# Kernel optimization log

Measured on AMD Instinct MI355X. Metric: run time of the kernel, lower is better.

## Reference

```python
import jax, jax.numpy as jnp
import numpy as np

D_IN, D_HIDDEN, DT_RANK = 768, 16, 48


def setup_inputs() -> dict:
    key = jax.random.key(0)
    ks = jax.random.split(key, 6)
    b, l, d, n, r = 2, 2048, D_IN, D_HIDDEN, DT_RANK
    p = 3 * n + 2 * d + 2 * r  # x_proj output width = 1680
    x = jax.random.normal(ks[0], (b, l, d), jnp.float32)
    z = jax.random.normal(ks[1], (b, d, l), jnp.float32)
    # A_log = log(repeat(arange(1, n+1), 'n -> d n'))
    A_log = jnp.log(jnp.broadcast_to(jnp.arange(1, n + 1, dtype=jnp.float32), (d, n)))
    D = jnp.ones((d,), jnp.float32)
    W_xproj = jax.random.normal(ks[2], (p, d), jnp.float32) / np.sqrt(d)
    W_dt = jax.random.normal(ks[3], (d, r), jnp.float32) / np.sqrt(r)
    # dt bias init: inverse-softplus of dt ~ LogUniform(1e-3, 1e-1)
    dt = jnp.exp(jax.random.uniform(ks[4], (d,)) * (np.log(0.1) - np.log(0.001)) + np.log(0.001))
    dt = jnp.clip(dt, 1e-4)
    b_dt = dt + jnp.log(-jnp.expm1(-dt))
    return dict(x=x, z=z, A_log=A_log, D=D, W_xproj=W_xproj, W_dt=W_dt, b_dt=b_dt)


def reference(x, z, A_log, D, W_xproj, W_dt, b_dt):
    b, l, d = x.shape
    n = A_log.shape[1]
    r = W_dt.shape[1]
    A = -jnp.exp(A_log)                      # (d, n)
    proj = x @ W_xproj.T                     # (b, l, 3n + 2d + 2r)
    Bm = proj[..., :n]                       # (b, l, n)  input matrix B
    Cm = proj[..., 2 * n:3 * n]              # (b, l, n)  output matrix C
    dt = proj[..., 3 * n + 2 * d:3 * n + 2 * d + r]   # (b, l, r)
    # NOTE: source adds dt_proj bias via the Linear AND again via delta_bias -> 2*b_dt
    delta = jax.nn.softplus(dt @ W_dt.T + 2.0 * b_dt)  # (b, l, d)
    dA = jnp.exp(delta[..., None] * A)                  # (b, l, d, n)
    dBu = (delta * x)[..., None] * Bm[:, :, None, :]    # (b, l, d, n)

    def step(h, inp):
        dA_t, dBu_t, C_t = inp
        h = dA_t * h + dBu_t                 # (b, d, n)
        return h, jnp.einsum('bdn,bn->bd', h, C_t)

    h0 = jnp.zeros((b, d, n), x.dtype)
    _, ys = jax.lax.scan(step, h0, (jnp.swapaxes(dA, 0, 1), jnp.swapaxes(dBu, 0, 1), jnp.swapaxes(Cm, 0, 1)))
    y = jnp.swapaxes(ys, 0, 1) + x * D       # (b, l, d)  + skip D*u
    zl = jnp.swapaxes(z, 1, 2)               # z is (b, d, l) -> (b, l, d)
    return y * (zl * jax.nn.sigmoid(zl))     # gate with silu(z)
```

## Files before the change

### kernel.cpp

```cpp
#include <hip/hip_runtime.h>
#include <math.h>

#define BATCH 2
#define LSEQ  2048
#define DIM   768
#define NST   16
#define RDT   48
#define BL    (BATCH*LSEQ)
#define NCHUNK 32
#define CLEN   (LSEQ/NCHUNK)
#define CPAD   68
#define NPACK  (CLEN/4)
#define LP4    (LSEQ/4)
#define L2E    1.4426950408889634f

typedef __attribute__((ext_vector_type(8))) short short8;
typedef __attribute__((ext_vector_type(4))) float float4e;

__device__ __forceinline__ ushort f2bf(float f) {
    union { float f; unsigned u; } v; v.f = f;
    unsigned u = v.u;
    u += 0x7fffu + ((u >> 16) & 1u);
    return (ushort)(u >> 16);
}

template <int CTRL>
__device__ __forceinline__ float dpp_add(float v) {
    const int s = __builtin_amdgcn_update_dpp(__float_as_int(v), __float_as_int(v),
                                              CTRL, 0xF, 0xF, false);
    return v + __int_as_float(s);
}

__global__ __launch_bounds__(256) void wpack_kernel(
        const float* __restrict__ Wx, const float* __restrict__ Wdt,
        ushort* __restrict__ Wbf, ushort* __restrict__ Wdtbf) {
    const int tid0 = blockIdx.x * 256 + threadIdx.x;
    for (int i = tid0; i < 80 * DIM; i += gridDim.x * 256) {
        const int j = i / DIM;
        const int k = i - j * DIM;
        const int row = (j < 16) ? j : ((j < 32) ? (j + 16) : (j + 1552));
        Wbf[i] = f2bf(Wx[(size_t)row * DIM + k]);
    }
    for (int i = tid0; i < DIM * 64; i += gridDim.x * 256) {
        const int dd = i >> 6;
        const int k = i & 63;
        Wdtbf[i] = (k < RDT) ? f2bf(Wdt[dd * RDT + k]) : (ushort)0;
    }
}

__global__ __launch_bounds__(320) void proj_gemm_kernel(
        const float* __restrict__ x, const ushort* __restrict__ Wbf,
        const ushort* __restrict__ Wdtbf, const float* __restrict__ bdt,
        float* __restrict__ Bpk, float* __restrict__ Cpk,
        float* __restrict__ deltaT, float* __restrict__ xT) {
    __shared__ float dtp_s[16 * 65];
    const int m0   = blockIdx.x * 16;
    const int nt   = threadIdx.x >> 6;
    const int lane = threadIdx.x & 63;
    const int col  = lane & 15;
    const int quad = lane >> 4;
    const int b  = m0 >> 11;
    const int t0 = m0 & 2047;

    for (int i = threadIdx.x; i < 16 * 65; i += 320) dtp_s[i] = 0.f;
    __syncthreads();

    const float* A  = x + (size_t)(m0 + col) * DIM + quad * 8;
    const short* Bw = (const short*)Wbf + (size_t)(nt * 16 + col) * DIM + quad * 8;

    float4e acc = {};
    #pragma unroll 4
    for (int kk = 0; kk < 24; ++kk) {
        const float4 a0 = *(const float4*)(A + kk * 32);
        const float4 a1 = *(const float4*)(A + kk * 32 + 4);
        short8 a;
        a[0] = (short)f2bf(a0.x); a[1] = (short)f2bf(a0.y);
        a[2] = (short)f2bf(a0.z); a[3] = (short)f2bf(a0.w);
        a[4] = (short)f2bf(a1.x); a[5] = (short)f2bf(a1.y);
        a[6] = (short)f2bf(a1.z); a[7] = (short)f2bf(a1.w);
        if (nt == 0) {
            const int dbase = kk * 32 + quad * 8;
            float* xc = xT + ((size_t)(b * DIM + dbase)) * LSEQ + t0 + col;
            xc[0 * LSEQ] = a0.x; xc[1 * LSEQ] = a0.y;
            xc[2 * LSEQ] = a0.z; xc[3 * LSEQ] = a0.w;
            xc[4 * LSEQ] = a1.x; xc[5 * LSEQ] = a1.y;
            xc[6 * LSEQ] = a1.z; xc[7 * LSEQ] = a1.w;
        }
        const short8 bf = *(const short8*)(Bw + kk * 32);
        acc = __builtin_amdgcn_mfma_f32_16x16x32_bf16(a, bf, acc, 0, 0, 0);
    }

    if (nt == 0) {
        ((float4*)Bpk)[((size_t)(b * LP4 + (t0 >> 2) + quad)) * NST + col] = *(float4*)&acc;
    } else if (nt == 1) {
        ((float4*)Cpk)[((size_t)(b * LP4 + (t0 >> 2) + quad)) * NST + col] = *(float4*)&acc;
    } else {
        #pragma unroll
        for (int r = 0; r < 4; ++r)
            dtp_s[(quad * 4 + r) * 65 + (nt - 2) * 16 + col] = acc[r];
    }
    __syncthreads();

    short8 da0, da1;
    #pragma unroll
    for (int j = 0; j < 8; ++j) {
        da0[j] = (short)f2bf(dtp_s[col * 65 + quad * 8 + j]);
        da1[j] = (short)f2bf(dtp_s[col * 65 + 32 + quad * 8 + j]);
    }
    for (int dt = nt; dt < 48; dt += 5) {
        const int d0 = dt * 16;
        const short8 b0 = *(const short8*)((const short*)Wdtbf + (size_t)(d0 + col) * 64 + quad * 8);
        const short8 b1 = *(const short8*)((const short*)Wdtbf + (size_t)(d0 + col) * 64 + 32 + quad * 8);
        float4e dacc = {};
        dacc = __builtin_amdgcn_mfma_f32_16x16x32_bf16(da0, b0, dacc, 0, 0, 0);
        dacc = __builtin_amdgcn_mfma_f32_16x16x32_bf16(da1, b1, dacc, 0, 0, 0);
        const float bb = 2.0f * bdt[d0 + col];
        float4 sp;
        {
            const float v0 = dacc[0] + bb, v1 = dacc[1] + bb;
            const float v2 = dacc[2] + bb, v3 = dacc[3] + bb;
            sp.x = (v0 > 20.f) ? v0 : __logf(1.f + __expf(v0));
            sp.y = (v1 > 20.f) ? v1 : __logf(1.f + __expf(v1));
            sp.z = (v2 > 20.f) ? v2 : __logf(1.f + __expf(v2));
            sp.w = (v3 > 20.f) ? v3 : __logf(1.f + __expf(v3));
        }
        *(float4*)(deltaT + ((size_t)(b * DIM + d0 + col)) * LSEQ + t0 + quad * 4) = sp;
    }
}

__global__ __launch_bounds__(512) void scan_kernel(
        const float* __restrict__ xT, const float* __restrict__ A_log,
        const float* __restrict__ Dp,
        const float* __restrict__ Bpk, const float* __restrict__ Cpk,
        const float* __restrict__ deltaT, float* __restrict__ yv) {
    __shared__ float sdel[NCHUNK * CPAD];
    __shared__ float sP[NCHUNK][NST];
    __shared__ float sq[NCHUNK][NST];

    const int tid = threadIdx.x;
    const int ch = blockIdx.x;
    const int b = ch / DIM;
    const int d = ch % DIM;
    const size_t row = (size_t)ch * LSEQ;

    {
        const float4 dv4 = ((const float4*)(deltaT + row))[tid];
        ((float4*)sdel)[(tid >> 4) * (CPAD / 4) + (tid & 15)] = dv4;
    }
    __syncthreads();

    const int g = tid >> 4;
    const int n = tid & 15;
    const float Aln2 = -__expf(A_log[d * NST + n]) * L2E;
    const float4* Bg = (const float4*)Bpk + ((size_t)(b * LP4 + g * NPACK) * NST + n);
    const float4* Cg = (const float4*)Cpk + ((size_t)(b * LP4 + g * NPACK) * NST + n);
    const float4* xr = (const float4*)(xT + row) + g * NPACK;
    const float* dchunk = sdel + g * CPAD;

    {
        float h = 0.f, Ptot = 1.f;
        float4 Bn_ = Bg[0], xn_ = xr[0];
        #pragma unroll 4
        for (int p = 0; p < NPACK; ++p) {
            const float4 B4 = Bn_, x4 = xn_;
            if (p < NPACK - 1) { Bn_ = Bg[(p + 1) * NST]; xn_ = xr[p + 1]; }
            const float4 dl = *(const float4*)(dchunk + 4 * p);
            const float u0 = dl.x * x4.x * B4.x, u1 = dl.y * x4.y * B4.y;
            const float u2 = dl.z * x4.z * B4.z, u3 = dl.w * x4.w * B4.w;
            const float e0  = __builtin_amdgcn_exp2f(Aln2 * dl.x);
            const float dA1 = __builtin_amdgcn_exp2f(Aln2 * dl.y);
            const float dA2 = __builtin_amdgcn_exp2f(Aln2 * dl.z);
            const float dA3 = __builtin_amdgcn_exp2f(Aln2 * dl.w);
            float s = u0;
            s = fmaf(dA1, s, u1); s = fmaf(dA2, s, u2); s = fmaf(dA3, s, u3);
            const float E3 = ((e0 * dA1) * (dA2 * dA3));
            h = fmaf(E3, h, s);
            Ptot *= E3;
        }
        sP[g][n] = Ptot;
        sq[g][n] = h;
    }
    __syncthreads();

    {
        float Pc = sP[g][n], qc = sq[g][n];
        #pragma unroll
        for (int s = 1; s < NCHUNK; s <<= 1) {
            float Pp = 1.f, qp = 0.f;
            if (g >= s) { Pp = sP[g - s][n]; qp = sq[g - s][n]; }
            __syncthreads();
            qc = fmaf(Pc, qp, qc);
            Pc *= Pp;
            sP[g][n] = Pc; sq[g][n] = qc;
            __syncthreads();
        }
    }

    {
        float h = (g == 0) ? 0.f : sq[g - 1][n];
        const float Dd = Dp[d];
        float4 Bn_ = Bg[0], Cn_ = Cg[0], xn_ = xr[0];
        #pragma unroll 4
        for (int p = 0; p < NPACK; ++p) {
            const float4 B4 = Bn_, C4 = Cn_, x4 = xn_;
            if (p < NPACK - 1) { Bn_ = Bg[(p + 1) * NST]; Cn_ = Cg[(p + 1) * NST]; xn_ = xr[p + 1]; }
            const float4 dl = *(const float4*)(dchunk + 4 * p);
            const float u0 = dl.x * x4.x * B4.x, u1 = dl.y * x4.y * B4.y;
            const float u2 = dl.z * x4.z * B4.z, u3 = dl.w * x4.w * B4.w;
            const float E0  = __builtin_amdgcn_exp2f(Aln2 * dl.x);
            const float dA1 = __builtin_amdgcn_exp2f(Aln2 * dl.y);
            const float dA2 = __builtin_amdgcn_exp2f(Aln2 * dl.z);
            const float dA3 = __builtin_amdgcn_exp2f(Aln2 * dl.w);
            const float E1 = E0 * dA1, E2 = E1 * dA2, E3 = E2 * dA3;
            const float s0 = u0;
            const float s1 = fmaf(dA1, s0, u1);
            const float s2 = fmaf(dA2, s1, u2);
            const float s3 = fmaf(dA3, s2, u3);
            const float h0 = fmaf(E0, h, s0);
            const float h1 = fmaf(E1, h, s1);
            const float h2 = fmaf(E2, h, s2);
            const float h3 = fmaf(E3, h, s3);
            h = h3;
            float p0 = h0 * C4.x, p1 = h1 * C4.y, p2 = h2 * C4.z, p3 = h3 * C4.w;
            p0 = dpp_add<0xB1>(p0); p0 = dpp_add<0x4E>(p0);
            p1 = dpp_add<0xB1>(p1); p1 = dpp_add<0x4E>(p1);
            p2 = dpp_add<0xB1>(p2); p2 = dpp_add<0x4E>(p2);
            p3 = dpp_add<0xB1>(p3); p3 = dpp_add<0x4E>(p3);
            float v = (n & 1) ? ((n & 2) ? p3 : p1) : ((n & 2) ? p2 : p0);
            v = dpp_add<0x124>(v);
            v = dpp_add<0x128>(v);
            if (n < 4) {
                const float xc = (n == 0) ? x4.x : (n == 1) ? x4.y : (n == 2) ? x4.z : x4.w;
                yv[row + g * CLEN + 4 * p + n] = fmaf(xc, Dd, v);
            }
        }
    }
}

__global__ __launch_bounds__(256) void xpose_out_kernel(
        const float* __restrict__ yv, const float* __restrict__ z,
        float* __restrict__ out) {
    __shared__ float tile[64 * 65];
    const int r0 = blockIdx.x * 64;
    const int c0 = blockIdx.y * 64;
    const int b  = blockIdx.z;
    const int tid = threadIdx.x;
    {
        const int c4 = tid & 15, rb = tid >> 4;
        #pragma unroll
        for (int rr = 0; rr < 4; ++rr) {
            const int row = rr * 16 + rb;
            const size_t gidx = ((size_t)b * DIM + r0 + row) * LSEQ + c0 + c4 * 4;
            const float4 v = *(const float4*)(yv + gidx);
            const float4 zv = *(const float4*)(z + gidx);
            tile[(c4 * 4 + 0) * 65 + row] = v.x * zv.x / (1.f + __expf(-zv.x));
            tile[(c4 * 4 + 1) * 65 + row] = v.y * zv.y / (1.f + __expf(-zv.y));
            tile[(c4 * 4 + 2) * 65 + row] = v.z * zv.z / (1.f + __expf(-zv.z));
            tile[(c4 * 4 + 3) * 65 + row] = v.w * zv.w / (1.f + __expf(-zv.w));
        }
    }
    __syncthreads();
    {
        const int t4 = tid & 15, dq = tid >> 4;
        #pragma unroll
        for (int pass = 0; pass < 4; ++pass) {
            const int ll = pass * 16 + dq;
            float4 v;
            v.x = tile[ll * 65 + t4 * 4 + 0];
            v.y = tile[ll * 65 + t4 * 4 + 1];
            v.z = tile[ll * 65 + t4 * 4 + 2];
            v.w = tile[ll * 65 + t4 * 4 + 3];
            *(float4*)(out + ((size_t)b * LSEQ + c0 + ll) * DIM + r0 + t4 * 4) = v;
        }
    }
}

extern "C" void kernel_launch(void* const* d_in, const int* in_sizes, int n_in,
                              void* d_out, int out_size, void* d_ws, size_t ws_size,
                              hipStream_t stream) {
    const float* x     = (const float*)d_in[0];
    const float* z     = (const float*)d_in[1];
    const float* A_log = (const float*)d_in[2];
    const float* D     = (const float*)d_in[3];
    const float* Wx    = (const float*)d_in[4];
    const float* Wdt   = (const float*)d_in[5];
    const float* bdt   = (const float*)d_in[6];
    float* out = (float*)d_out;

    float* ws     = (float*)d_ws;
    float* Bpk    = ws;
    float* Cpk    = Bpk + (size_t)BATCH * LP4 * NST * 4;
    float* deltaT = Cpk + (size_t)BATCH * LP4 * NST * 4;
    float* xT     = deltaT + (size_t)BATCH * DIM * LSEQ;
    float* yv     = xT;
    ushort* Wbf   = (ushort*)(xT + (size_t)BATCH * DIM * LSEQ);
    ushort* Wdtbf = Wbf + (size_t)80 * DIM;

    hipLaunchKernelGGL(wpack_kernel, dim3(64), dim3(256), 0, stream,
                       Wx, Wdt, Wbf, Wdtbf);
    hipLaunchKernelGGL(proj_gemm_kernel, dim3(BL / 16), dim3(320), 0, stream,
                       x, Wbf, Wdtbf, bdt, Bpk, Cpk, deltaT, xT);
    hipLaunchKernelGGL(scan_kernel, dim3(BATCH * DIM), dim3(512), 0, stream,
                       xT, A_log, D, Bpk, Cpk, deltaT, yv);
    hipLaunchKernelGGL(xpose_out_kernel, dim3(DIM / 64, LSEQ / 64, BATCH), dim3(256), 0, stream,
                       yv, z, out);
}
```

Baseline: 152.5 us.

## Fuse weight bf16 packing into projection GEMM, spread xT writes, precompute delta*x

Removes the separate weight-packing kernel. The projection GEMM now reads fp32 weights directly and converts them to bf16 in registers, which saves one launch and a round trip through global memory but repeats the conversion in every block. The transposed-x stores, previously done by wave 0 alone, are split across all five waves by k-range to balance the store load. The scan kernel precomputes delta*x into a new shared buffer so both scan passes skip one multiply and the x global load in the first pass, at the cost of extra LDS.

```diff
diff --git a/kernel.cpp b/kernel.cpp
--- a/kernel.cpp
+++ b/kernel.cpp
@@ -31,26 +31,18 @@
     return v + __int_as_float(s);
 }
 
-__global__ __launch_bounds__(256) void wpack_kernel(
-        const float* __restrict__ Wx, const float* __restrict__ Wdt,
-        ushort* __restrict__ Wbf, ushort* __restrict__ Wdtbf) {
-    const int tid0 = blockIdx.x * 256 + threadIdx.x;
-    for (int i = tid0; i < 80 * DIM; i += gridDim.x * 256) {
-        const int j = i / DIM;
-        const int k = i - j * DIM;
-        const int row = (j < 16) ? j : ((j < 32) ? (j + 16) : (j + 1552));
-        Wbf[i] = f2bf(Wx[(size_t)row * DIM + k]);
-    }
-    for (int i = tid0; i < DIM * 64; i += gridDim.x * 256) {
-        const int dd = i >> 6;
-        const int k = i & 63;
-        Wdtbf[i] = (k < RDT) ? f2bf(Wdt[dd * RDT + k]) : (ushort)0;
-    }
+__device__ __forceinline__ short8 cvt8(float4 a, float4 b) {
+    short8 r;
+    r[0] = (short)f2bf(a.x); r[1] = (short)f2bf(a.y);
+    r[2] = (short)f2bf(a.z); r[3] = (short)f2bf(a.w);
+    r[4] = (short)f2bf(b.x); r[5] = (short)f2bf(b.y);
+    r[6] = (short)f2bf(b.z); r[7] = (short)f2bf(b.w);
+    return r;
 }
 
 __global__ __launch_bounds__(320) void proj_gemm_kernel(
-        const float* __restrict__ x, const ushort* __restrict__ Wbf,
-        const ushort* __restrict__ Wdtbf, const float* __restrict__ bdt,
+        const float* __restrict__ x, const float* __restrict__ Wx,
+        const float* __restrict__ Wdt, const float* __restrict__ bdt,
         float* __restrict__ Bpk, float* __restrict__ Cpk,
         float* __restrict__ deltaT, float* __restrict__ xT) {
     __shared__ float dtp_s[16 * 65];
@@ -65,20 +57,20 @@
     for (int i = threadIdx.x; i < 16 * 65; i += 320) dtp_s[i] = 0.f;
     __syncthreads();
 
+    const int j80  = nt * 16 + col;
+    const int wrow = (j80 < 16) ? j80 : ((j80 < 32) ? (j80 + 16) : (j80 + 1552));
     const float* A  = x + (size_t)(m0 + col) * DIM + quad * 8;
-    const short* Bw = (const short*)Wbf + (size_t)(nt * 16 + col) * DIM + quad * 8;
+    const float* Wr = Wx + (size_t)wrow * DIM + quad * 8;
+
+    const int kklo = nt * 5;
+    const int kkhi = (nt == 4) ? 24 : (kklo + 5);
 
     float4e acc = {};
     #pragma unroll 4
     for (int kk = 0; kk < 24; ++kk) {
         const float4 a0 = *(const float4*)(A + kk * 32);
         const float4 a1 = *(const float4*)(A + kk * 32 + 4);
-        short8 a;
-        a[0] = (short)f2bf(a0.x); a[1] = (short)f2bf(a0.y);
-        a[2] = (short)f2bf(a0.z); a[3] = (short)f2bf(a0.w);
-        a[4] = (short)f2bf(a1.x); a[5] = (short)f2bf(a1.y);
-        a[6] = (short)f2bf(a1.z); a[7] = (short)f2bf(a1.w);
-        if (nt == 0) {
+        if (kk >= kklo && kk < kkhi) {
             const int dbase = kk * 32 + quad * 8;
             float* xc = xT + ((size_t)(b * DIM + dbase)) * LSEQ + t0 + col;
             xc[0 * LSEQ] = a0.x; xc[1 * LSEQ] = a0.y;
@@ -86,8 +78,10 @@
             xc[4 * LSEQ] = a1.x; xc[5 * LSEQ] = a1.y;
             xc[6 * LSEQ] = a1.z; xc[7 * LSEQ] = a1.w;
         }
-        const short8 bf = *(const short8*)(Bw + kk * 32);
-        acc = __builtin_amdgcn_mfma_f32_16x16x32_bf16(a, bf, acc, 0, 0, 0);
+        const float4 w0 = *(const float4*)(Wr + kk * 32);
+        const float4 w1 = *(const float4*)(Wr + kk * 32 + 4);
+        acc = __builtin_amdgcn_mfma_f32_16x16x32_bf16(cvt8(a0, a1), cvt8(w0, w1),
+                                                      acc, 0, 0, 0);
     }
 
     if (nt == 0) {
@@ -109,8 +103,13 @@
     }
     for (int dt = nt; dt < 48; dt += 5) {
         const int d0 = dt * 16;
-        const short8 b0 = *(const short8*)((const short*)Wdtbf + (size_t)(d0 + col) * 64 + quad * 8);
-        const short8 b1 = *(const short8*)((const short*)Wdtbf + (size_t)(d0 + col) * 64 + 32 + quad * 8);
+        const float* wd = Wdt + (size_t)(d0 + col) * RDT;
+        const short8 b0 = cvt8(*(const float4*)(wd + quad * 8),
+                               *(const float4*)(wd + quad * 8 + 4));
+        short8 b1 = {};
+        if (quad < 2)
+            b1 = cvt8(*(const float4*)(wd + 32 + quad * 8),
+                      *(const float4*)(wd + 32 + quad * 8 + 4));
         float4e dacc = {};
         dacc = __builtin_amdgcn_mfma_f32_16x16x32_bf16(da0, b0, dacc, 0, 0, 0);
         dacc = __builtin_amdgcn_mfma_f32_16x16x32_bf16(da1, b1, dacc, 0, 0, 0);
@@ -134,6 +133,7 @@
         const float* __restrict__ Bpk, const float* __restrict__ Cpk,
         const float* __restrict__ deltaT, float* __restrict__ yv) {
     __shared__ float sdel[NCHUNK * CPAD];
+    __shared__ float sdlx[NCHUNK * CPAD];
     __shared__ float sP[NCHUNK][NST];
     __shared__ float sq[NCHUNK][NST];
 
@@ -145,7 +145,11 @@
 
     {
         const float4 dv4 = ((const float4*)(deltaT + row))[tid];
-        ((float4*)sdel)[(tid >> 4) * (CPAD / 4) + (tid & 15)] = dv4;
+        const float4 xv4 = ((const float4*)(xT + row))[tid];
+        const int sidx = (tid >> 4) * (CPAD / 4) + (tid & 15);
+        ((float4*)sdel)[sidx] = dv4;
+        ((float4*)sdlx)[sidx] = make_float4(dv4.x * xv4.x, dv4.y * xv4.y,
+                                            dv4.z * xv4.z, dv4.w * xv4.w);
     }
     __syncthreads();
 
@@ -156,17 +160,19 @@
     const float4* Cg = (const float4*)Cpk + ((size_t)(b * LP4 + g * NPACK) * NST + n);
     const float4* xr = (const float4*)(xT + row) + g * NPACK;
     const float* dchunk = sdel + g * CPAD;
+    const float* uchunk = sdlx + g * CPAD;
 
     {
         float h = 0.f, Ptot = 1.f;
-        float4 Bn_ = Bg[0], xn_ = xr[0];
+        float4 Bn_ = Bg[0];
         #pragma unroll 4
         for (int p = 0; p < NPACK; ++p) {
-            const float4 B4 = Bn_, x4 = xn_;
-            if (p < NPACK - 1) { Bn_ = Bg[(p + 1) * NST]; xn_ = xr[p + 1]; }
+            const float4 B4 = Bn_;
+            if (p < NPACK - 1) Bn_ = Bg[(p + 1) * NST];
             const float4 dl = *(const float4*)(dchunk + 4 * p);
-            const float u0 = dl.x * x4.x * B4.x, u1 = dl.y * x4.y * B4.y;
-            const float u2 = dl.z * x4.z * B4.z, u3 = dl.w * x4.w * B4.w;
+            const float4 ux = *(const float4*)(uchunk + 4 * p);
+            const float u0 = ux.x * B4.x, u1 = ux.y * B4.y;
+            const float u2 = ux.z * B4.z, u3 = ux.w * B4.w;
             const float e0  = __builtin_amdgcn_exp2f(Aln2 * dl.x);
             const float dA1 = __builtin_amdgcn_exp2f(Aln2 * dl.y);
             const float dA2 = __builtin_amdgcn_exp2f(Aln2 * dl.z);
@@ -205,8 +211,9 @@
             const float4 B4 = Bn_, C4 = Cn_, x4 = xn_;
             if (p < NPACK - 1) { Bn_ = Bg[(p + 1) * NST]; Cn_ = Cg[(p + 1) * NST]; xn_ = xr[p + 1]; }
             const float4 dl = *(const float4*)(dchunk + 4 * p);
-            const float u0 = dl.x * x4.x * B4.x, u1 = dl.y * x4.y * B4.y;
-            const float u2 = dl.z * x4.z * B4.z, u3 = dl.w * x4.w * B4.w;
+            const float4 ux = *(const float4*)(uchunk + 4 * p);
+            const float u0 = ux.x * B4.x, u1 = ux.y * B4.y;
+            const float u2 = ux.z * B4.z, u3 = ux.w * B4.w;
             const float E0  = __builtin_amdgcn_exp2f(Aln2 * dl.x);
             const float dA1 = __builtin_amdgcn_exp2f(Aln2 * dl.y);
             const float dA2 = __builtin_amdgcn_exp2f(Aln2 * dl.z);
@@ -293,13 +300,9 @@
     float* deltaT = Cpk + (size_t)BATCH * LP4 * NST * 4;
     float* xT     = deltaT + (size_t)BATCH * DIM * LSEQ;
     float* yv     = xT;
-    ushort* Wbf   = (ushort*)(xT + (size_t)BATCH * DIM * LSEQ);
-    ushort* Wdtbf = Wbf + (size_t)80 * DIM;
-
-    hipLaunchKernelGGL(wpack_kernel, dim3(64), dim3(256), 0, stream,
-                       Wx, Wdt, Wbf, Wdtbf);
+
     hipLaunchKernelGGL(proj_gemm_kernel, dim3(BL / 16), dim3(320), 0, stream,
-                       x, Wbf, Wdtbf, bdt, Bpk, Cpk, deltaT, xT);
+                       x, Wx, Wdt, bdt, Bpk, Cpk, deltaT, xT);
     hipLaunchKernelGGL(scan_kernel, dim3(BATCH * DIM), dim3(512), 0, stream,
                        xT, A_log, D, Bpk, Cpk, deltaT, yv);
     hipLaunchKernelGGL(xpose_out_kernel, dim3(DIM / 64, LSEQ / 64, BATCH), dim3(256), 0, stream,
```

New measurement: 147.6 us. -3.2%, faster.
